# Optimization experiments

Measured on AMD Instinct MI355X. Metric: run time of the kernel, lower is better.

## Reference

```python
import jax, jax.numpy as jnp
import numpy as np

B, D, N, M = 24, 128, 2048, 2048
DROPOUT_P = 0.1

def setup_inputs() -> dict:
    key = jax.random.key(0)
    kc, kq, kw = jax.random.split(key, 3)
    C = jax.random.normal(kc, (B, D, N), dtype=jnp.float32)
    Q = jax.random.normal(kq, (B, D, M), dtype=jnp.float32)
    W = jax.random.normal(kw, (B, 1, 3 * D), dtype=jnp.float32)
    return {"C": C, "Q": Q, "W": W}

def reference(C, Q, W):
    d = C.shape[1]
    # W = [Wq | Wc | Wm], each [B, d]; S[b,i,j] = Wq.Q_j + Wc.C_i + (Wm*C_i).Q_j
    Wq = W[:, 0, :d]
    Wc = W[:, 0, d:2 * d]
    Wm = W[:, 0, 2 * d:]
    sq = jnp.einsum('bd,bdm->bm', Wq, Q)                 # [B, m]
    sc = jnp.einsum('bd,bdn->bn', Wc, C)                 # [B, n]
    st = jnp.einsum('bdn,bd,bdm->bnm', C, Wm, Q)         # trilinear term [B, n, m]
    S = st + sc[:, :, None] + sq[:, None, :]             # [B, n, m]
    S1 = jax.nn.softmax(S, axis=2)                       # over query positions
    S2 = jax.nn.softmax(S, axis=1)                       # over context positions
    A = jnp.einsum('bdm,bnm->bdn', Q, S1)                # Q @ S1^T  -> [B, d, n]
    T = jnp.einsum('bnm,bkm->bnk', S1, S2)               # S1 @ S2^T -> [B, n, n]
    Bt = jnp.einsum('bdn,bkn->bdk', C, T)                # C @ T^T   -> [B, d, n]
    out = jnp.concatenate([C, A, C * A, C * Bt], axis=1) # [B, 4d, n]
    # dropout (training=True, p=0.1), deterministic key for reproducibility
    keep = jax.random.bernoulli(jax.random.key(42), 1.0 - DROPOUT_P, out.shape)
    out = jnp.where(keep, out / (1.0 - DROPOUT_P), 0.0)
    return out
```

## Files before the change

### kernel.cpp

```cpp
#include <hip/hip_runtime.h>
#include <cstdint>
#include <cstddef>

constexpr int Bn = 24;
constexpr int Dd = 128;
constexpr int Nn = 2048;
constexpr int DN = Dd * Nn;
constexpr int NIT = Nn / 64;
constexpr float INV_KEEP = 1.0f / 0.9f;

typedef __attribute__((ext_vector_type(8))) short short8;
typedef __attribute__((ext_vector_type(16))) float floatx16;

union U8 { uint32_t u[4]; short8 v; uint4 q; };

__device__ __forceinline__ uint32_t f2bf(float f) {
  uint32_t u = __builtin_bit_cast(uint32_t, f);
  return (u + 0x7fffu + ((u >> 16) & 1u)) >> 16;
}
__device__ __forceinline__ float bf2f(uint32_t h) {
  return __builtin_bit_cast(float, h << 16);
}

__device__ __forceinline__ floatx16 MFMA(short8 a, short8 b, floatx16 c) {
  return __builtin_amdgcn_mfma_f32_32x32x16_bf16(a, b, c, 0, 0, 0);
}

__device__ __forceinline__ void gload_lds16(const void* g, void* l) {
  __builtin_amdgcn_global_load_lds(
      (const __attribute__((address_space(1))) void*)g,
      (__attribute__((address_space(3))) void*)l, 16, 0, 0);
}

__device__ __forceinline__ uint32_t rotl32(uint32_t x, int r) {
  return (x << r) | (x >> (32 - r));
}
__device__ __forceinline__ void tf2x32(uint32_t& x0, uint32_t& x1) {
  const uint32_t k0 = 0u, k1 = 42u, k2 = 0x1BD11BDAu ^ 0u ^ 42u;
  x0 += k0; x1 += k1;
#define TFR(r) { x0 += x1; x1 = rotl32(x1, (r)); x1 ^= x0; }
  TFR(13) TFR(15) TFR(26) TFR(6)   x0 += k1; x1 += k2 + 1u;
  TFR(17) TFR(29) TFR(16) TFR(24)  x0 += k2; x1 += k0 + 2u;
  TFR(13) TFR(15) TFR(26) TFR(6)   x0 += k0; x1 += k1 + 3u;
  TFR(17) TFR(29) TFR(16) TFR(24)  x0 += k1; x1 += k2 + 4u;
  TFR(13) TFR(15) TFR(26) TFR(6)   x0 += k2; x1 += k0 + 5u;
#undef TFR
}
__device__ __forceinline__ bool keep_flag(uint32_t j) {
  uint32_t x0 = 0u, x1 = j;
  tf2x32(x0, x1);
  return ((x0 ^ x1) >> 9) < 7549747u;
}

__global__ void scq_kernel(const float* __restrict__ Cp, const float* __restrict__ Qp,
                           const float* __restrict__ Wp,
                           float* __restrict__ sc, float* __restrict__ sq) {
  const int z = blockIdx.z;
  const int b = blockIdx.y;
  const int n = blockIdx.x * 256 + threadIdx.x;
  const float* X = z ? Qp : Cp;
  const float* Wb = Wp + b * 384 + (z ? 0 : 128);
  const float* Xb = X + (size_t)b * DN + n;
  float acc = 0.f;
#pragma unroll 8
  for (int d = 0; d < Dd; ++d) acc = fmaf(Wb[d], Xb[(size_t)d * Nn], acc);
  (z ? sq : sc)[b * Nn + n] = acc;
}

__global__ __launch_bounds__(256) void bias_adjust_kernel(float* __restrict__ sc,
                                                          float* __restrict__ sq) {
  __shared__ float red[256];
  const int tid = threadIdx.x;
  float* v = ((blockIdx.x & 1) ? sq : sc) + (size_t)(blockIdx.x >> 1) * Nn;
  float m = -__builtin_inff();
#pragma unroll
  for (int i = 0; i < 8; ++i) m = fmaxf(m, v[tid + 256 * i]);
  red[tid] = m;
  __syncthreads();
  for (int s = 128; s > 0; s >>= 1) {
    if (tid < s) red[tid] = fmaxf(red[tid], red[tid + s]);
    __syncthreads();
  }
  const float mm = red[0];
#pragma unroll
  for (int i = 0; i < 8; ++i) v[tid + 256 * i] -= mm;
}

__global__ __launch_bounds__(256) void cvt_kernel(const float* __restrict__ Cp,
                                                  const float* __restrict__ Qp,
                                                  float* __restrict__ outp) {
  const size_t i = ((size_t)blockIdx.x * 256 + threadIdx.x) * 8;
  const int b = (int)(i >> 18);
  const int rem = (int)(i & (DN - 1));
  uint16_t* d0 = (uint16_t*)(outp + (size_t)b * 4 * DN);
  {
    const float4 a = *(const float4*)(Cp + i);
    const float4 c = *(const float4*)(Cp + i + 4);
    U8 t;
    t.u[0] = f2bf(a.x) | (f2bf(a.y) << 16);
    t.u[1] = f2bf(a.z) | (f2bf(a.w) << 16);
    t.u[2] = f2bf(c.x) | (f2bf(c.y) << 16);
    t.u[3] = f2bf(c.z) | (f2bf(c.w) << 16);
    *(uint4*)(d0 + rem) = t.q;
  }
  {
    const float4 a = *(const float4*)(Qp + i);
    const float4 c = *(const float4*)(Qp + i + 4);
    U8 t;
    t.u[0] = f2bf(a.x) | (f2bf(a.y) << 16);
    t.u[1] = f2bf(a.z) | (f2bf(a.w) << 16);
    t.u[2] = f2bf(c.x) | (f2bf(c.y) << 16);
    t.u[3] = f2bf(c.z) | (f2bf(c.w) << 16);
    *(uint4*)(d0 + DN + rem) = t.q;
  }
}

__global__ __launch_bounds__(256) void split_kernel(const float* __restrict__ Cp,
                                                    const float* __restrict__ Qp,
                                                    float* __restrict__ outp) {
  __shared__ float T[64 * 129];
  const int tid = threadIdx.x;
  const int nt = blockIdx.x, src = blockIdx.y, b = blockIdx.z;
  const float* X = (src ? Qp : Cp) + (size_t)b * DN;
  float* outb = outp + (size_t)b * 4 * DN;
  uint16_t* dsth = (uint16_t*)(outb + (size_t)(src ? 1 : 3) * DN);
  uint16_t* dstl = dsth + DN;
  const int n = nt * 64 + (tid & 63);
  const int dg0 = (tid >> 6) * 32;
#pragma unroll
  for (int r = 0; r < 32; ++r)
    T[(tid & 63) * 129 + dg0 + r] = X[(size_t)(dg0 + r) * Nn + n];
  __syncthreads();
#pragma unroll
  for (int r = 0; r < 4; ++r) {
    const int item = tid + 256 * r;
    const int row = item >> 4;
    const int ch = item & 15;
    const float* tp = T + row * 129 + ch * 8;
    U8 H, L;
#pragma unroll
    for (int e = 0; e < 4; ++e) {
      const float va = tp[2 * e], vb = tp[2 * e + 1];
      const uint32_t ha = f2bf(va), hb = f2bf(vb);
      H.u[e] = ha | (hb << 16);
      L.u[e] = f2bf(va - bf2f(ha)) | (f2bf(vb - bf2f(hb)) << 16);
    }
    const size_t o = (size_t)(nt * 64 + row) * 128 + ch * 8;
    *(uint4*)(dsth + o) = H.q;
    *(uint4*)(dstl + o) = L.q;
  }
}

template<bool DUAL>
__global__ __launch_bounds__(256, 2) void pass_kernel(
    const float* __restrict__ Cp, const float* __restrict__ Qp,
    const float* __restrict__ Wp, float* __restrict__ outp,
    const float* __restrict__ scp, const float* __restrict__ sqp) {
  __shared__ uint16_t Bs[2][2][64 * 128];
  __shared__ uint16_t EsS[2][64 * 64];

  const int tid = threadIdx.x;
  const int lane = tid & 63;
  const int w = tid >> 6;
  const int xh = w >> 1, yh = w & 1;
  const int lh = lane >> 5, l31 = lane & 31;

  const int bid = blockIdx.x;
  const int jj = bid >> 3;
  const int b = (bid & 7) * 3 + (jj >> 5);
  const int x0 = (jj & 31) * 64;

  const float* Cb = Cp + (size_t)b * DN;
  const float* Qb = Qp + (size_t)b * DN;
  float* outb = outp + (size_t)b * 4 * DN;
  const float* Wmb = Wp + b * 384 + 256;

  const float* Asrc = DUAL ? Cb : Qb;
  const uint16_t* V1 = (const uint16_t*)outb + (DUAL ? DN : 0);
  const uint16_t* V2 = DUAL ? (const uint16_t*)(outb + 2 * DN) : nullptr;
  const uint16_t* BTh = (const uint16_t*)(outb + (size_t)(DUAL ? 1 : 3) * DN);
  const uint16_t* BTl = BTh + DN;
  const float* byp = (DUAL ? sqp : scp) + b * Nn;

  auto stage = [&](int bn, int y0n) {
#pragma unroll
    for (int j = 0; j < 4; ++j) {
      const int s = w * 256 + j * 64 + lane;
      const int y = s >> 4;
      const int cs = ((s & 15) ^ (y & 15)) * 8;
      const size_t gof = (size_t)(y0n + y) * 128 + cs;
      const int lof = (w * 256 + j * 64) * 8;
      gload_lds16(BTh + gof, &Bs[bn][0][lof]);
      gload_lds16(BTl + gof, &Bs[bn][1][lof]);
    }
  };

  short8 xfh[8], xfl[8];
  float sig2 = 0.f;
  {
    const int xg = x0 + xh * 32 + l31;
#pragma unroll
    for (int ks = 0; ks < 8; ++ks) {
      U8 th, tl;
#pragma unroll
      for (int e = 0; e < 4; ++e) {
        const int d0 = ks * 16 + lh * 8 + e * 2;
        const float va = Asrc[(size_t)d0 * Nn + xg] * Wmb[d0];
        const float vb = Asrc[(size_t)(d0 + 1) * Nn + xg] * Wmb[d0 + 1];
        sig2 += va * va + vb * vb;
        const uint32_t ha = f2bf(va), hb = f2bf(vb);
        th.u[e] = ha | (hb << 16);
        tl.u[e] = f2bf(va - bf2f(ha)) | (f2bf(vb - bf2f(hb)) << 16);
      }
      xfh[ks] = th.v; xfl[ks] = tl.v;
    }
  }
  sig2 += __shfl_xor(sig2, 32);
  const float c3 = 3.0f * sqrtf(sig2);

  float s_run = 0.f;

  floatx16 aA0, aA1, aB0, aB1;
#pragma unroll
  for (int r = 0; r < 16; ++r) { aA0[r] = 0.f; aA1[r] = 0.f; }
  if constexpr (DUAL) {
#pragma unroll
    for (int r = 0; r < 16; ++r) { aB0[r] = 0.f; aB1[r] = 0.f; }
  }

  const int yrow = yh * 32 + l31;
  const int xl = xh * 32 + l31;
  const int dloc = w * 32 + l31;
  const int ybias = yh * 32 + 4 * lh;

  auto pv_step = [&](int pb, int y0p) {
    short8 vf1[4], vf2[4];
    {
      const uint16_t* v1p = V1 + (size_t)dloc * Nn + y0p + lh * 8;
#pragma unroll
      for (int ks = 0; ks < 4; ++ks)
        vf1[ks] = *(const short8*)(v1p + ks * 16);
      if constexpr (DUAL) {
        const uint16_t* v2p = V2 + (size_t)dloc * Nn + y0p + lh * 8;
#pragma unroll
        for (int ks = 0; ks < 4; ++ks)
          vf2[ks] = *(const short8*)(v2p + ks * 16);
      }
    }
#pragma unroll
    for (int ks = 0; ks < 4; ++ks) {
      const int sw = ((2 * ks + lh) ^ (l31 & 7)) * 8;
      const short8 e0 = *(const short8*)(&EsS[pb][l31 * 64 + sw]);
      const short8 e1 = *(const short8*)(&EsS[pb][(32 + l31) * 64 + sw]);
      aA0 = MFMA(vf1[ks], e0, aA0);
      aA1 = MFMA(vf1[ks], e1, aA1);
      if constexpr (DUAL) {
        aB0 = MFMA(vf2[ks], e0, aB0);
        aB1 = MFMA(vf2[ks], e1, aB1);
      }
    }
  };

  stage(0, 0);

#pragma unroll 1
  for (int it = 0; it < NIT; ++it) {
    const int y0i = it * 64;
    const int cur = it & 1;

    __syncthreads();

    if (it + 1 < NIT) stage(cur ^ 1, y0i + 64);

    float4 bv[4];
#pragma unroll
    for (int gq = 0; gq < 4; ++gq)
      bv[gq] = *(const float4*)(byp + y0i + ybias + 8 * gq);

    const uint16_t* brH = &Bs[cur][0][yrow * 128];
    const uint16_t* brL = &Bs[cur][1][yrow * 128];
    floatx16 Sa, Sb, Sc;
#pragma unroll
    for (int r = 0; r < 16; ++r) { Sa[r] = 0.f; Sb[r] = 0.f; Sc[r] = 0.f; }
#pragma unroll
    for (int ks = 0; ks < 8; ++ks) {
      const int ch = ((2 * ks + lh) ^ (yrow & 15)) * 8;
      const short8 bh = *(const short8*)(brH + ch);
      const short8 bl = *(const short8*)(brL + ch);
      Sa = MFMA(bh, xfh[ks], Sa);
      Sb = MFMA(bl, xfh[ks], Sb);
      Sc = MFMA(bh, xfl[ks], Sc);
    }

    if (it > 0) pv_step(cur ^ 1, y0i - 64);

    float Sv[16];
#pragma unroll
    for (int gq = 0; gq < 4; ++gq) {
      Sv[4 * gq + 0] = Sa[4 * gq + 0] + Sb[4 * gq + 0] + Sc[4 * gq + 0] + (bv[gq].x - c3);
      Sv[4 * gq + 1] = Sa[4 * gq + 1] + Sb[4 * gq + 1] + Sc[4 * gq + 1] + (bv[gq].y - c3);
      Sv[4 * gq + 2] = Sa[4 * gq + 2] + Sb[4 * gq + 2] + Sc[4 * gq + 2] + (bv[gq].z - c3);
      Sv[4 * gq + 3] = Sa[4 * gq + 3] + Sb[4 * gq + 3] + Sc[4 * gq + 3] + (bv[gq].w - c3);
    }
#pragma unroll
    for (int gq = 0; gq < 4; ++gq) {
      const float e0 = __expf(Sv[4 * gq + 0]);
      const float e1 = __expf(Sv[4 * gq + 1]);
      const float e2 = __expf(Sv[4 * gq + 2]);
      const float e3 = __expf(Sv[4 * gq + 3]);
      s_run += (e0 + e1) + (e2 + e3);
      uint2 pk;
      pk.x = f2bf(e0) | (f2bf(e1) << 16);
      pk.y = f2bf(e2) | (f2bf(e3) << 16);
      const int c = 4 * yh + gq;
      *(uint2*)(&EsS[cur][xl * 64 + ((c ^ (xl & 7)) * 8 + 4 * lh)]) = pk;
    }
  }

  __syncthreads();
  pv_step((NIT - 1) & 1, (NIT - 1) * 64);

  s_run += __shfl_xor(s_run, 32);
  float* spart = (float*)(&EsS[0][0]);
  if (lh == 0) spart[yh * 64 + xl] = s_run;
  __syncthreads();
  const float inv0 = 1.0f / (spart[l31] + spart[64 + l31]);
  const float inv1 = 1.0f / (spart[32 + l31] + spart[96 + l31]);
#pragma unroll
  for (int r = 0; r < 16; ++r) {
    const int d = w * 32 + (r & 3) + 8 * (r >> 2) + 4 * lh;
    if constexpr (DUAL) {
      float* oa = outb + 3 * DN + (size_t)d * Nn + x0;
      oa[l31] = aA0[r] * inv0;
      oa[32 + l31] = aA1[r] * inv1;
      float* ob = (d < 64) ? (outb + (size_t)d * Nn + x0)
                           : (outb + 2 * DN + DN / 2 + (size_t)(d - 64) * Nn + x0);
      ob[l31] = aB0[r] * inv0;
      ob[32 + l31] = aB1[r] * inv1;
    } else {
      uint16_t* ou = (uint16_t*)(outb + 2 * DN) + (size_t)d * Nn + x0;
      ou[l31] = (uint16_t)f2bf(aA0[r] * inv0);
      ou[32 + l31] = (uint16_t)f2bf(aA1[r] * inv1);
    }
  }
}

__global__ void epilogue_kernel(const float* __restrict__ Cp, float* __restrict__ outp) {
  const int g = blockIdx.x * 256 + threadIdx.x;
  const int b = g >> 18;
  const int rem = g & ((1 << 18) - 1);
  const int dd = rem >> 11;
  const float c = Cp[g];
  const int base = (b << 20) + rem;
  const float a = outp[base + (3 << 18)];
  const float bt = outp[base + ((dd >= 64) ? (2 << 18) : 0)];
  const float vals[4] = {c, a, c * a, c * bt};
#pragma unroll
  for (int s = 0; s < 4; ++s) {
    const int j = base + (s << 18);
    outp[j] = keep_flag((uint32_t)j) ? vals[s] * INV_KEEP : 0.0f;
  }
}

extern "C" void kernel_launch(void* const* d_in, const int* in_sizes, int n_in,
                              void* d_out, int out_size, void* d_ws, size_t ws_size,
                              hipStream_t stream) {
  (void)in_sizes; (void)n_in; (void)out_size; (void)ws_size;
  const float* C = (const float*)d_in[0];
  const float* Q = (const float*)d_in[1];
  const float* W = (const float*)d_in[2];
  float* out = (float*)d_out;
  float* ws = (float*)d_ws;

  float* sc = ws;
  float* sq = ws + Bn * Nn;

  cvt_kernel<<<(Bn * DN) / (256 * 8), 256, 0, stream>>>(C, Q, out);
  split_kernel<<<dim3(Nn / 64, 2, Bn), 256, 0, stream>>>(C, Q, out);
  scq_kernel<<<dim3(Nn / 256, Bn, 2), 256, 0, stream>>>(C, Q, W, sc, sq);
  bias_adjust_kernel<<<2 * Bn, 256, 0, stream>>>(sc, sq);
  pass_kernel<false><<<dim3(Nn / 64 * Bn), 256, 0, stream>>>(C, Q, W, out, sc, sq);
  pass_kernel<true><<<dim3(Nn / 64 * Bn), 256, 0, stream>>>(C, Q, W, out, sc, sq);
  epilogue_kernel<<<(Bn * DN) / 256, 256, 0, stream>>>(C, out);
}
```

Before: 606.4 us.

## Prefetch V fragments and bias a stage ahead; merge split-bf16 accumulators

Global loads of the V1/V2 fragments for the PV step are now issued one iteration early, right after the previous PV MFMAs, so their latency overlaps the exp/pack work and the next S computation. The bias vector for the next tile is also prefetched at the end of each iteration. The three separate S accumulators (hi*hi, lo*hi, hi*lo) are folded into one chained accumulator, which cuts accumulator registers but serializes the MFMA dependency chain. Keeping the prefetched fragments live across the loop raises register pressure.

```diff
diff --git a/kernel.cpp b/kernel.cpp
--- a/kernel.cpp
+++ b/kernel.cpp
@@ -233,20 +233,10 @@
   const int dloc = w * 32 + l31;
   const int ybias = yh * 32 + 4 * lh;
 
-  auto pv_step = [&](int pb, int y0p) {
-    short8 vf1[4], vf2[4];
-    {
-      const uint16_t* v1p = V1 + (size_t)dloc * Nn + y0p + lh * 8;
-#pragma unroll
-      for (int ks = 0; ks < 4; ++ks)
-        vf1[ks] = *(const short8*)(v1p + ks * 16);
-      if constexpr (DUAL) {
-        const uint16_t* v2p = V2 + (size_t)dloc * Nn + y0p + lh * 8;
-#pragma unroll
-        for (int ks = 0; ks < 4; ++ks)
-          vf2[ks] = *(const short8*)(v2p + ks * 16);
-      }
-    }
+  short8 vf1[4], vf2[4];
+  float4 bvc[4];
+
+  auto consume_pv = [&](int pb) {
 #pragma unroll
     for (int ks = 0; ks < 4; ++ks) {
       const int sw = ((2 * ks + lh) ^ (l31 & 7)) * 8;
@@ -260,8 +250,23 @@
       }
     }
   };
+  auto issue_v = [&](int y0p) {
+    const uint16_t* v1p = V1 + (size_t)dloc * Nn + y0p + lh * 8;
+#pragma unroll
+    for (int ks = 0; ks < 4; ++ks)
+      vf1[ks] = *(const short8*)(v1p + ks * 16);
+    if constexpr (DUAL) {
+      const uint16_t* v2p = V2 + (size_t)dloc * Nn + y0p + lh * 8;
+#pragma unroll
+      for (int ks = 0; ks < 4; ++ks)
+        vf2[ks] = *(const short8*)(v2p + ks * 16);
+    }
+  };
 
   stage(0, 0);
+#pragma unroll
+  for (int gq = 0; gq < 4; ++gq)
+    bvc[gq] = *(const float4*)(byp + ybias + 8 * gq);
 
 #pragma unroll 1
   for (int it = 0; it < NIT; ++it) {
@@ -272,42 +277,31 @@
 
     if (it + 1 < NIT) stage(cur ^ 1, y0i + 64);
 
-    float4 bv[4];
-#pragma unroll
-    for (int gq = 0; gq < 4; ++gq)
-      bv[gq] = *(const float4*)(byp + y0i + ybias + 8 * gq);
-
     const uint16_t* brH = &Bs[cur][0][yrow * 128];
     const uint16_t* brL = &Bs[cur][1][yrow * 128];
-    floatx16 Sa, Sb, Sc;
-#pragma unroll
-    for (int r = 0; r < 16; ++r) { Sa[r] = 0.f; Sb[r] = 0.f; Sc[r] = 0.f; }
+    floatx16 S;
+#pragma unroll
+    for (int r = 0; r < 16; ++r) S[r] = 0.f;
 #pragma unroll
     for (int ks = 0; ks < 8; ++ks) {
       const int ch = ((2 * ks + lh) ^ (yrow & 15)) * 8;
       const short8 bh = *(const short8*)(brH + ch);
       const short8 bl = *(const short8*)(brL + ch);
-      Sa = MFMA(bh, xfh[ks], Sa);
-      Sb = MFMA(bl, xfh[ks], Sb);
-      Sc = MFMA(bh, xfl[ks], Sc);
-    }
-
-    if (it > 0) pv_step(cur ^ 1, y0i - 64);
-
-    float Sv[16];
+      S = MFMA(bh, xfh[ks], S);
+      S = MFMA(bl, xfh[ks], S);
+      S = MFMA(bh, xfl[ks], S);
+    }
+
+    if (it > 0) consume_pv(cur ^ 1);
+
+    issue_v(y0i);
+
 #pragma unroll
     for (int gq = 0; gq < 4; ++gq) {
-      Sv[4 * gq + 0] = Sa[4 * gq + 0] + Sb[4 * gq + 0] + Sc[4 * gq + 0] + (bv[gq].x - c3);
-      Sv[4 * gq + 1] = Sa[4 * gq + 1] + Sb[4 * gq + 1] + Sc[4 * gq + 1] + (bv[gq].y - c3);
-      Sv[4 * gq + 2] = Sa[4 * gq + 2] + Sb[4 * gq + 2] + Sc[4 * gq + 2] + (bv[gq].z - c3);
-      Sv[4 * gq + 3] = Sa[4 * gq + 3] + Sb[4 * gq + 3] + Sc[4 * gq + 3] + (bv[gq].w - c3);
-    }
-#pragma unroll
-    for (int gq = 0; gq < 4; ++gq) {
-      const float e0 = __expf(Sv[4 * gq + 0]);
-      const float e1 = __expf(Sv[4 * gq + 1]);
-      const float e2 = __expf(Sv[4 * gq + 2]);
-      const float e3 = __expf(Sv[4 * gq + 3]);
+      const float e0 = __expf(S[4 * gq + 0] + (bvc[gq].x - c3));
+      const float e1 = __expf(S[4 * gq + 1] + (bvc[gq].y - c3));
+      const float e2 = __expf(S[4 * gq + 2] + (bvc[gq].z - c3));
+      const float e3 = __expf(S[4 * gq + 3] + (bvc[gq].w - c3));
       s_run += (e0 + e1) + (e2 + e3);
       uint2 pk;
       pk.x = f2bf(e0) | (f2bf(e1) << 16);
@@ -315,10 +309,16 @@
       const int c = 4 * yh + gq;
       *(uint2*)(&EsS[cur][xl * 64 + ((c ^ (xl & 7)) * 8 + 4 * lh)]) = pk;
     }
+
+    if (it + 1 < NIT) {
+#pragma unroll
+      for (int gq = 0; gq < 4; ++gq)
+        bvc[gq] = *(const float4*)(byp + y0i + 64 + ybias + 8 * gq);
+    }
   }
 
   __syncthreads();
-  pv_step((NIT - 1) & 1, (NIT - 1) * 64);
+  consume_pv((NIT - 1) & 1);
 
   s_run += __shfl_xor(s_run, 32);
   float* spart = (float*)(&EsS[0][0]);
```

Result: faster. 544.4 us (-10.2%).
